# Optimization experiments

Hardware: AMD Instinct MI355X
Metric: run time of the kernel (lower is better)

Reference implementation:

```python
import jax, jax.numpy as jnp
import numpy as np

# dims
B, S, H = 2, 256, 1024          # batch, global seq, global hidden
BH, NH = 384, 8                  # byte_hidden, num heads
HD = BH // NH                    # head dim = 48
P = 4                            # num_global_proj (seed byte positions)
S_C = 12                         # byte decode steps (= target.shape[2])
L = 4                            # num_byte_decoder_layers
V = 258                          # byte vocab (256 bytes + pad 256 + eos 257)
T = P + S_C
EOS = 257
SCALE = 1.0 / np.sqrt(HD)


def setup_inputs() -> dict:
    key = jax.random.key(0)
    ks = jax.random.split(key, 12)
    w = lambda k, shp: jax.random.normal(k, shp, jnp.float32) * 0.02
    return {
        "x": jax.random.normal(ks[0], (B, S, H), jnp.float32),
        "target": jax.random.randint(ks[1], (B, S, S_C), 0, V),
        "Wproj": w(ks[2], (H, P * BH)),
        "attn_norm": jnp.ones((L, BH), jnp.float32),
        "Wq": w(ks[3], (L, BH, BH)),
        "Wk": w(ks[4], (L, BH, BH)),
        "Wv": w(ks[5], (L, BH, BH)),
        "Wo": w(ks[6], (L, BH, BH)),
        "ffn_norm": jnp.ones((L, BH), jnp.float32),
        "W1": w(ks[7], (L, BH, 4 * BH)),
        "W2": w(ks[8], (L, 4 * BH, BH)),
        "Wlm": w(ks[9], (BH, V)),
    }


def _rms(x, g):
    return x * jax.lax.rsqrt(jnp.mean(x * x, -1, keepdims=True) + 1e-5) * g


def _block(x, kc, vc, pos, an, Wq, Wk, Wv, Wo, fn, W1, W2, causal):
    # x: [N, Lq, BH]; kc/vc: [N, T, NH, HD] KV caches; pos: static write offset
    N, Lq, _ = x.shape
    h = _rms(x, an)
    q = (h @ Wq).reshape(N, Lq, NH, HD)
    k = (h @ Wk).reshape(N, Lq, NH, HD)
    v = (h @ Wv).reshape(N, Lq, NH, HD)
    kc = jax.lax.dynamic_update_slice(kc, k, (0, pos, 0, 0))
    vc = jax.lax.dynamic_update_slice(vc, v, (0, pos, 0, 0))
    nk = pos + Lq
    sc = jnp.einsum('nqhd,nkhd->nhqk', q, kc[:, :nk]) * SCALE
    if causal:
        mask = jnp.arange(nk)[None, :] <= (pos + jnp.arange(Lq))[:, None]
        sc = jnp.where(mask[None, None], sc, jnp.float32(-1e30))
    p = jax.nn.softmax(sc, axis=-1)
    o = jnp.einsum('nhqk,nkhd->nqhd', p, vc[:, :nk]).reshape(N, Lq, BH)
    x = x + o @ Wo
    x = x + jax.nn.gelu(_rms(x, fn) @ W1, approximate=False) @ W2
    return x, kc, vc


def _forward(x, Wproj, attn_norm, Wq, Wk, Wv, Wo, ffn_norm, W1, W2, Wlm):
    N = B * S
    x0 = (x.reshape(N, H) @ Wproj).reshape(N, P, BH)
    x_out = jnp.zeros((N, T, BH), x0.dtype).at[:, :P].set(x0)
    kc = [jnp.zeros((N, T, NH, HD), x0.dtype) for _ in range(L)]
    vc = [jnp.zeros((N, T, NH, HD), x0.dtype) for _ in range(L)]
    finished = jnp.zeros((N,), bool)
    for i in range(S_C):
        if i == 0:
            pos, xi, causal = 0, x_out[:, :P], True          # prefill seed bytes
        else:
            pos, xi, causal = P + i - 1, x_out[:, P + i - 1:P + i], False  # decode 1 token
        for l in range(L):
            xi, kc[l], vc[l] = _block(xi, kc[l], vc[l], pos,
                                      attn_norm[l], Wq[l], Wk[l], Wv[l], Wo[l],
                                      ffn_norm[l], W1[l], W2[l], causal)
        gen = xi[:, -1]                                       # [N, BH]
        unf = ~finished
        # scatter only unfinished streams back (finished stay zero, as in torch)
        x_out = x_out.at[:, P + i].set(jnp.where(unf[:, None], gen, jnp.float32(0.0)))
        finished = finished | (unf & (jnp.argmax(gen, -1) == EOS))
    return x_out.reshape(B, S, T, BH)[:, :, P:, :] @ Wlm      # [B,S,S_C,V]


def reference(x, target, Wproj, attn_norm, Wq, Wk, Wv, Wo, ffn_norm, W1, W2, Wlm):
    del target  # only sets S_c (static here)
    return _forward(x, Wproj, attn_norm, Wq, Wk, Wv, Wo, ffn_norm, W1, W2, Wlm)
```

## Files before the change

kernel.cpp:

```cpp
#include <hip/hip_runtime.h>
#include <hip/hip_bf16.h>


constexpr int H_IN  = 1024;
constexpr int BH    = 384;
constexpr int NH    = 8;
constexpr int HD    = 48;
constexpr int PP    = 4;
constexpr int S_CNT = 12;
constexpr int NL    = 4;
constexpr int NV    = 258;
constexpr int TT    = 16;
constexpr int NSEQ  = 512;
constexpr int EOS_I = 257;
constexpr int NTH   = 768;
constexpr float RSCALE = 0.14433756729740646f;

typedef _Float16 h2 __attribute__((ext_vector_type(2)));
typedef _Float16 h8 __attribute__((ext_vector_type(8)));

union W16 { h8 v8; h2 h[4]; _Float16 e[8]; };

template<int N> struct IC { static constexpr int value = N; };

__device__ __forceinline__ float fdot2(h2 a, h2 b, float c) {
#if __has_builtin(__builtin_amdgcn_fdot2)
  return __builtin_amdgcn_fdot2(a, b, c, false);
#else
  return c + (float)a.x * (float)b.x + (float)a.y * (float)b.y;
#endif
}

__global__ __launch_bounds__(256)
void pack8_kernel(const float* __restrict__ src, h8* __restrict__ dst, int C) {
  int c  = blockIdx.x * 256 + threadIdx.x;
  int j8 = blockIdx.y;
  if (c < C) {
    h8 v;
    #pragma unroll
    for (int r = 0; r < 8; r++) v[r] = (_Float16)src[(size_t)(8 * j8 + r) * C + c];
    dst[(size_t)j8 * C + c] = v;
  }
}

__global__ __launch_bounds__(NTH)
void decoder_kernel(const float* __restrict__ x,
                    const h8* __restrict__ Wproj8,
                    const float* __restrict__ attn_norm,
                    const h8* __restrict__ Wq8,
                    const h8* __restrict__ Wk8,
                    const h8* __restrict__ Wv8,
                    const h8* __restrict__ Wo8,
                    const float* __restrict__ ffn_norm,
                    const h8* __restrict__ W18,
                    const h8* __restrict__ W28,
                    const h8* __restrict__ Wlm8,
                    float* __restrict__ out,
                    _Float16* __restrict__ kbuf,
                    _Float16* __restrict__ vbuf)
{
  __shared__ float xs[2][4][BH];
  __shared__ __align__(16) _Float16 hh[2][4][BH];
  __shared__ __align__(16) _Float16 qh[2][4][BH];
  __shared__ __align__(16) _Float16 oh[2][4][BH];
  __shared__ __align__(16) _Float16 xh[2][H_IN];
  __shared__ __align__(16) _Float16 genh[2][BH];
  __shared__ float sc[2][NH][4][TT];
  __shared__ union Scr {
    float qkvp[3][2][4][BH];
    float wop[2][4][BH];
    struct { __align__(16) _Float16 f1h[2][4][4*BH];
             float w2p[2][4][BH]; } ffn;
  } scr;
  __shared__ float redsum[4][12];
  __shared__ float redv[12];
  __shared__ int   redi[12];
  __shared__ int   amx[2];
  __shared__ int   fin[2];

  const int tid = threadIdx.x;
  const int kg  = tid / BH;
  const int col = tid - kg * BH;
  const int sq  = kg;
  const int wid = tid >> 6;
  const int seq0 = blockIdx.x * 2;

  if (tid < 2) fin[tid] = 0;

  for (int s = 0; s < 2; s++) {
    const size_t base = (size_t)(seq0 + s) * H_IN;
    for (int j = tid; j < H_IN; j += NTH) xh[s][j] = (_Float16)x[base + j];
  }
  __syncthreads();
  {
    float acc[2][2] = {};
    for (int j8 = 0; j8 < H_IN / 8; j8 += 4) {
      W16 w0[4], w1[4];
      #pragma unroll
      for (int u = 0; u < 4; u++) {
        w0[u].v8 = Wproj8[(size_t)(j8 + u) * (PP * BH) + tid];
        w1[u].v8 = Wproj8[(size_t)(j8 + u) * (PP * BH) + tid + NTH];
      }
      #pragma unroll
      for (int u = 0; u < 4; u++)
        #pragma unroll
        for (int s = 0; s < 2; s++) {
          W16 hv; hv.v8 = *(const h8*)&xh[s][(j8 + u) * 8];
          #pragma unroll
          for (int r = 0; r < 4; r++) {
            acc[s][0] = fdot2(hv.h[r], w0[u].h[r], acc[s][0]);
            acc[s][1] = fdot2(hv.h[r], w1[u].h[r], acc[s][1]);
          }
        }
    }
    const int m0 = tid / BH, cc = tid % BH;
    for (int s = 0; s < 2; s++) {
      xs[s][m0][cc]     = acc[s][0];
      xs[s][m0 + 2][cc] = acc[s][1];
    }
  }
  __syncthreads();

  auto layers = [&](auto ntc, int pos, bool causal) {
    constexpr int NT = decltype(ntc)::value;
    const int nk = pos + NT;
    for (int l = 0; l < NL; l++) {
      {
        #pragma unroll
        for (int tok = 0; tok < NT; tok++) {
          float r = xs[sq][tok][col]; r *= r;
          #pragma unroll
          for (int off = 32; off; off >>= 1) r += __shfl_down(r, off, 64);
          if ((tid & 63) == 0) redsum[tok][wid] = r;
        }
        __syncthreads();
        const int b = sq * 6;
        #pragma unroll
        for (int tok = 0; tok < NT; tok++) {
          float ss = redsum[tok][b] + redsum[tok][b+1] + redsum[tok][b+2] +
                     redsum[tok][b+3] + redsum[tok][b+4] + redsum[tok][b+5];
          float sca = rsqrtf(ss * (1.0f / BH) + 1e-5f);
          hh[sq][tok][col] = (_Float16)(xs[sq][tok][col] * sca * attn_norm[l * BH + col]);
        }
        __syncthreads();
      }
      {
        const size_t wb = ((size_t)l * 48 + kg * 24) * BH + col;
        float aq[2][NT] = {}, ak[2][NT] = {}, av[2][NT] = {};
        for (int j8 = 0; j8 < 24; j8 += 4) {
          W16 wq[4], wk[4], wv[4];
          #pragma unroll
          for (int u = 0; u < 4; u++) {
            wq[u].v8 = Wq8[wb + (size_t)(j8 + u) * BH];
            wk[u].v8 = Wk8[wb + (size_t)(j8 + u) * BH];
            wv[u].v8 = Wv8[wb + (size_t)(j8 + u) * BH];
          }
          #pragma unroll
          for (int u = 0; u < 4; u++)
            #pragma unroll
            for (int s = 0; s < 2; s++)
              #pragma unroll
              for (int tok = 0; tok < NT; tok++) {
                W16 hv; hv.v8 = *(const h8*)&hh[s][tok][(kg * 24 + j8 + u) * 8];
                #pragma unroll
                for (int r = 0; r < 4; r++) {
                  aq[s][tok] = fdot2(hv.h[r], wq[u].h[r], aq[s][tok]);
                  ak[s][tok] = fdot2(hv.h[r], wk[u].h[r], ak[s][tok]);
                  av[s][tok] = fdot2(hv.h[r], wv[u].h[r], av[s][tok]);
                }
              }
        }
        if (kg == 1) {
          #pragma unroll
          for (int s = 0; s < 2; s++)
            #pragma unroll
            for (int tok = 0; tok < NT; tok++) {
              scr.qkvp[0][s][tok][col] = aq[s][tok];
              scr.qkvp[1][s][tok][col] = ak[s][tok];
              scr.qkvp[2][s][tok][col] = av[s][tok];
            }
        }
        __syncthreads();
        if (kg == 0) {
          #pragma unroll
          for (int s = 0; s < 2; s++) {
            const size_t cb = (((size_t)(seq0 + s) * NL + l) * TT + pos) * BH + col;
            #pragma unroll
            for (int tok = 0; tok < NT; tok++) {
              qh[s][tok][col] = (_Float16)(aq[s][tok] + scr.qkvp[0][s][tok][col]);
              kbuf[cb + (size_t)tok * BH] = (_Float16)(ak[s][tok] + scr.qkvp[1][s][tok][col]);
              vbuf[cb + (size_t)tok * BH] = (_Float16)(av[s][tok] + scr.qkvp[2][s][tok][col]);
            }
          }
        }
        __syncthreads();
      }
      {
        const int nu = 2 * NH * NT * nk;
        if (tid < nu) {
          int s = tid / (NH * NT * nk), r = tid % (NH * NT * nk);
          int h = r / (NT * nk); int r2 = r % (NT * nk);
          int qi = r2 / nk, j = r2 % nk;
          float d;
          if (causal && j > pos + qi) d = -1e30f;
          else {
            const h8* kp8 = (const h8*)(kbuf + (((size_t)(seq0 + s) * NL + l) * TT + j) * BH + h * HD);
            W16 kk[6];
            #pragma unroll
            for (int c = 0; c < 6; c++) kk[c].v8 = kp8[c];
            d = 0.f;
            #pragma unroll
            for (int c = 0; c < 6; c++)
              #pragma unroll
              for (int e = 0; e < 8; e++)
                d += (float)qh[s][qi][h * HD + c * 8 + e] * (float)kk[c].e[e];
            d *= RSCALE;
          }
          sc[s][h][qi][j] = d;
        }
      }
      __syncthreads();
      {
        const int nr = 2 * NH * NT;
        if (tid < nr) {
          int s = tid / (NH * NT), r = tid % (NH * NT);
          int h = r / NT, qi = r % NT;
          float m = -3.0e38f;
          for (int j = 0; j < nk; j++) m = fmaxf(m, sc[s][h][qi][j]);
          float den = 0.f;
          for (int j = 0; j < nk; j++) {
            float e = expf(sc[s][h][qi][j] - m);
            sc[s][h][qi][j] = e; den += e;
          }
          float inv = 1.0f / den;
          for (int j = 0; j < nk; j++) sc[s][h][qi][j] *= inv;
        }
      }
      __syncthreads();
      {
        const size_t vb = (((size_t)(seq0 + sq) * NL + l) * TT) * BH + col;
        const int h = col / HD;
        #pragma unroll
        for (int tok = 0; tok < NT; tok++) {
          float acc = 0.f;
          int j = 0;
          for (; j + 4 <= nk; j += 4) {
            float v0 = (float)vbuf[vb + (size_t)(j + 0) * BH];
            float v1 = (float)vbuf[vb + (size_t)(j + 1) * BH];
            float v2 = (float)vbuf[vb + (size_t)(j + 2) * BH];
            float v3 = (float)vbuf[vb + (size_t)(j + 3) * BH];
            acc += sc[sq][h][tok][j] * v0 + sc[sq][h][tok][j+1] * v1 +
                   sc[sq][h][tok][j+2] * v2 + sc[sq][h][tok][j+3] * v3;
          }
          for (; j < nk; j++)
            acc += sc[sq][h][tok][j] * (float)vbuf[vb + (size_t)j * BH];
          oh[sq][tok][col] = (_Float16)acc;
        }
      }
      __syncthreads();
      {
        const size_t wb = ((size_t)l * 48 + kg * 24) * BH + col;
        float ao[2][NT] = {};
        for (int j8 = 0; j8 < 24; j8 += 8) {
          W16 w[8];
          #pragma unroll
          for (int u = 0; u < 8; u++) w[u].v8 = Wo8[wb + (size_t)(j8 + u) * BH];
          #pragma unroll
          for (int u = 0; u < 8; u++)
            #pragma unroll
            for (int s = 0; s < 2; s++)
              #pragma unroll
              for (int tok = 0; tok < NT; tok++) {
                W16 hv; hv.v8 = *(const h8*)&oh[s][tok][(kg * 24 + j8 + u) * 8];
                #pragma unroll
                for (int r = 0; r < 4; r++)
                  ao[s][tok] = fdot2(hv.h[r], w[u].h[r], ao[s][tok]);
              }
        }
        if (kg == 1) {
          #pragma unroll
          for (int s = 0; s < 2; s++)
            #pragma unroll
            for (int tok = 0; tok < NT; tok++) scr.wop[s][tok][col] = ao[s][tok];
        }
        __syncthreads();
        if (kg == 0) {
          #pragma unroll
          for (int s = 0; s < 2; s++)
            #pragma unroll
            for (int tok = 0; tok < NT; tok++)
              xs[s][tok][col] += ao[s][tok] + scr.wop[s][tok][col];
        }
        __syncthreads();
      }
      {
        #pragma unroll
        for (int tok = 0; tok < NT; tok++) {
          float r = xs[sq][tok][col]; r *= r;
          #pragma unroll
          for (int off = 32; off; off >>= 1) r += __shfl_down(r, off, 64);
          if ((tid & 63) == 0) redsum[tok][wid] = r;
        }
        __syncthreads();
        const int b = sq * 6;
        #pragma unroll
        for (int tok = 0; tok < NT; tok++) {
          float ss = redsum[tok][b] + redsum[tok][b+1] + redsum[tok][b+2] +
                     redsum[tok][b+3] + redsum[tok][b+4] + redsum[tok][b+5];
          float sca = rsqrtf(ss * (1.0f / BH) + 1e-5f);
          hh[sq][tok][col] = (_Float16)(xs[sq][tok][col] * sca * ffn_norm[l * BH + col]);
        }
        __syncthreads();
      }
      {
        float a1[2][NT][2] = {};
        for (int j8 = 0; j8 < 48; j8 += 4) {
          W16 w0[4], w1[4];
          #pragma unroll
          for (int u = 0; u < 4; u++) {
            w0[u].v8 = W18[((size_t)(l * 48 + j8 + u)) * (4 * BH) + tid];
            w1[u].v8 = W18[((size_t)(l * 48 + j8 + u)) * (4 * BH) + tid + NTH];
          }
          #pragma unroll
          for (int u = 0; u < 4; u++)
            #pragma unroll
            for (int s = 0; s < 2; s++)
              #pragma unroll
              for (int t = 0; t < NT; t++) {
                W16 hv; hv.v8 = *(const h8*)&hh[s][t][(j8 + u) * 8];
                #pragma unroll
                for (int r = 0; r < 4; r++) {
                  a1[s][t][0] = fdot2(hv.h[r], w0[u].h[r], a1[s][t][0]);
                  a1[s][t][1] = fdot2(hv.h[r], w1[u].h[r], a1[s][t][1]);
                }
              }
        }
        #pragma unroll
        for (int s = 0; s < 2; s++)
          #pragma unroll
          for (int t = 0; t < NT; t++) {
            float z0 = a1[s][t][0], z1 = a1[s][t][1];
            scr.ffn.f1h[s][t][tid]       = (_Float16)(0.5f * z0 * (1.0f + erff(z0 * 0.7071067811865476f)));
            scr.ffn.f1h[s][t][tid + NTH] = (_Float16)(0.5f * z1 * (1.0f + erff(z1 * 0.7071067811865476f)));
          }
        __syncthreads();
        {
          float a2[2][NT] = {};
          for (int j8 = 0; j8 < 96; j8 += 8) {
            W16 w[8];
            #pragma unroll
            for (int u = 0; u < 8; u++)
              w[u].v8 = W28[((size_t)(l * 192 + kg * 96 + j8 + u)) * BH + col];
            #pragma unroll
            for (int u = 0; u < 8; u++)
              #pragma unroll
              for (int s = 0; s < 2; s++)
                #pragma unroll
                for (int t = 0; t < NT; t++) {
                  W16 fv; fv.v8 = *(const h8*)&scr.ffn.f1h[s][t][(kg * 96 + j8 + u) * 8];
                  #pragma unroll
                  for (int r = 0; r < 4; r++)
                    a2[s][t] = fdot2(fv.h[r], w[u].h[r], a2[s][t]);
                }
          }
          if (kg == 1) {
            #pragma unroll
            for (int s = 0; s < 2; s++)
              #pragma unroll
              for (int t = 0; t < NT; t++) scr.ffn.w2p[s][t][col] = a2[s][t];
          }
          __syncthreads();
          if (kg == 0) {
            #pragma unroll
            for (int s = 0; s < 2; s++)
              #pragma unroll
              for (int t = 0; t < NT; t++)
                xs[s][t][col] += a2[s][t] + scr.ffn.w2p[s][t][col];
          }
          __syncthreads();
        }
      }
    }
  };

  for (int i = 0; i < S_CNT; i++) {
    int grow;
    if (i == 0) { layers(IC<4>{}, 0, true);           grow = 3; }
    else        { layers(IC<1>{}, PP + i - 1, false); grow = 0; }

    {
      float v = xs[sq][grow][col]; int idx = col;
      #pragma unroll
      for (int off = 32; off; off >>= 1) {
        float v2 = __shfl_down(v, off, 64); int i2 = __shfl_down(idx, off, 64);
        if (v2 > v || (v2 == v && i2 < idx)) { v = v2; idx = i2; }
      }
      if ((tid & 63) == 0) { redv[wid] = v; redi[wid] = idx; }
      __syncthreads();
      if (col == 0) {
        const int b = sq * 6;
        float bv = redv[b]; int bi = redi[b];
        for (int w = 1; w < 6; w++)
          if (redv[b + w] > bv || (redv[b + w] == bv && redi[b + w] < bi)) {
            bv = redv[b + w]; bi = redi[b + w];
          }
        amx[sq] = bi;
      }
      genh[sq][col] = (_Float16)xs[sq][grow][col];
      __syncthreads();
    }
    if (col < NV) {
      float acc = 0.f;
      for (int j8 = 0; j8 < 48; j8 += 8) {
        W16 w[8];
        #pragma unroll
        for (int u = 0; u < 8; u++) w[u].v8 = Wlm8[(size_t)(j8 + u) * NV + col];
        #pragma unroll
        for (int u = 0; u < 8; u++) {
          W16 gv; gv.v8 = *(const h8*)&genh[sq][(j8 + u) * 8];
          #pragma unroll
          for (int r = 0; r < 4; r++) acc = fdot2(gv.h[r], w[u].h[r], acc);
        }
      }
      out[((size_t)(seq0 + sq) * S_CNT + i) * NV + col] = fin[sq] ? 0.0f : acc;
    }
    __syncthreads();
    {
      float gv = xs[sq][grow][col];
      xs[sq][0][col] = fin[sq] ? 0.0f : gv;
    }
    __syncthreads();
    if (tid < 2 && amx[tid] == EOS_I) fin[tid] = 1;
    __syncthreads();
  }
}

extern "C" void kernel_launch(void* const* d_in, const int* in_sizes, int n_in,
                              void* d_out, int out_size, void* d_ws, size_t ws_size,
                              hipStream_t stream) {
  const float* x     = (const float*)d_in[0];
  const float* Wproj = (const float*)d_in[2];
  const float* an    = (const float*)d_in[3];
  const float* Wq    = (const float*)d_in[4];
  const float* Wk    = (const float*)d_in[5];
  const float* Wv    = (const float*)d_in[6];
  const float* Wo    = (const float*)d_in[7];
  const float* fn    = (const float*)d_in[8];
  const float* W1    = (const float*)d_in[9];
  const float* W2    = (const float*)d_in[10];
  const float* Wlm   = (const float*)d_in[11];
  float* out = (float*)d_out;
  (void)ws_size; (void)in_sizes; (void)n_in; (void)out_size;

  h8* w = (h8*)d_ws;
  const int n_proj = (H_IN / 8) * (PP * BH);
  const int n_qkvo = NL * (BH / 8) * BH;
  const int n_w1   = NL * (BH / 8) * (4 * BH);
  const int n_w2   = NL * (4 * BH / 8) * BH;
  const int n_lm   = (BH / 8) * NV;
  h8* Wproj_p = w;  w += n_proj;
  h8* Wq_p    = w;  w += n_qkvo;
  h8* Wk_p    = w;  w += n_qkvo;
  h8* Wv_p    = w;  w += n_qkvo;
  h8* Wo_p    = w;  w += n_qkvo;
  h8* W1_p    = w;  w += n_w1;
  h8* W2_p    = w;  w += n_w2;
  h8* Wlm_p   = w;  w += n_lm;
  const size_t kv_elems = (size_t)NSEQ * NL * TT * BH;
  _Float16* kbuf = (_Float16*)w;
  _Float16* vbuf = kbuf + kv_elems;

  auto pack = [&](const float* src, h8* dst, int R, int C) {
    dim3 grid((C + 255) / 256, R / 8);
    pack8_kernel<<<grid, 256, 0, stream>>>(src, dst, C);
  };
  pack(Wproj, Wproj_p, H_IN,        PP * BH);
  pack(Wq,    Wq_p,    NL * BH,     BH);
  pack(Wk,    Wk_p,    NL * BH,     BH);
  pack(Wv,    Wv_p,    NL * BH,     BH);
  pack(Wo,    Wo_p,    NL * BH,     BH);
  pack(W1,    W1_p,    NL * BH,     4 * BH);
  pack(W2,    W2_p,    NL * 4 * BH, BH);
  pack(Wlm,   Wlm_p,   BH,          NV);

  decoder_kernel<<<NSEQ / 2, NTH, 0, stream>>>(
      x, Wproj_p, an, Wq_p, Wk_p, Wv_p, Wo_p, fn, W1_p, W2_p, Wlm_p, out, kbuf, vbuf);
}
```

Before: 2.433 ms.

## Fold RMSNorm gains into packed weights and defer normalization scale past matmuls

The RMSNorm gain vectors are multiplied into the fp16-packed Wq/Wk/Wv/W1 rows at pack time. The per-token rsqrt scale is applied after the QKV and W1 matmuls instead of before, and the attention 1/sqrt(d) factor is folded into q. Sum-of-squares reductions are fused into the residual updates, which removes two norm phases and their barriers per layer. The sequential tail (argmax, LM head, feedback) is merged into fewer sync phases. Because the unnormalized residual is now cast to fp16 before the matmul, precision and overflow risk goes up if activations grow large.

```diff
diff --git a/kernel.cpp b/kernel.cpp
--- a/kernel.cpp
+++ b/kernel.cpp
@@ -32,13 +32,18 @@
 }
 
 __global__ __launch_bounds__(256)
-void pack8_kernel(const float* __restrict__ src, h8* __restrict__ dst, int C) {
+void pack8_kernel(const float* __restrict__ src, const float* __restrict__ g,
+                  h8* __restrict__ dst, int C) {
   int c  = blockIdx.x * 256 + threadIdx.x;
   int j8 = blockIdx.y;
   if (c < C) {
     h8 v;
     #pragma unroll
-    for (int r = 0; r < 8; r++) v[r] = (_Float16)src[(size_t)(8 * j8 + r) * C + c];
+    for (int r = 0; r < 8; r++) {
+      int row = 8 * j8 + r;
+      float s = g ? g[row] : 1.0f;
+      v[r] = (_Float16)(src[(size_t)row * C + c] * s);
+    }
     dst[(size_t)j8 * C + c] = v;
   }
 }
@@ -46,12 +51,10 @@
 __global__ __launch_bounds__(NTH)
 void decoder_kernel(const float* __restrict__ x,
                     const h8* __restrict__ Wproj8,
-                    const float* __restrict__ attn_norm,
                     const h8* __restrict__ Wq8,
                     const h8* __restrict__ Wk8,
                     const h8* __restrict__ Wv8,
                     const h8* __restrict__ Wo8,
-                    const float* __restrict__ ffn_norm,
                     const h8* __restrict__ W18,
                     const h8* __restrict__ W28,
                     const h8* __restrict__ Wlm8,
@@ -60,22 +63,20 @@
                     _Float16* __restrict__ vbuf)
 {
   __shared__ float xs[2][4][BH];
-  __shared__ __align__(16) _Float16 hh[2][4][BH];
+  __shared__ __align__(16) _Float16 xh[2][4][BH];
   __shared__ __align__(16) _Float16 qh[2][4][BH];
   __shared__ __align__(16) _Float16 oh[2][4][BH];
-  __shared__ __align__(16) _Float16 xh[2][H_IN];
-  __shared__ __align__(16) _Float16 genh[2][BH];
   __shared__ float sc[2][NH][4][TT];
-  __shared__ union Scr {
+  __shared__ __align__(16) union Scr {
     float qkvp[3][2][4][BH];
     float wop[2][4][BH];
     struct { __align__(16) _Float16 f1h[2][4][4*BH];
              float w2p[2][4][BH]; } ffn;
+    __align__(16) _Float16 xin[2][H_IN];
   } scr;
-  __shared__ float redsum[4][12];
+  __shared__ float redsq[2][4][6];
   __shared__ float redv[12];
   __shared__ int   redi[12];
-  __shared__ int   amx[2];
   __shared__ int   fin[2];
 
   const int tid = threadIdx.x;
@@ -83,13 +84,14 @@
   const int col = tid - kg * BH;
   const int sq  = kg;
   const int wid = tid >> 6;
+  const int w6  = wid % 6;
   const int seq0 = blockIdx.x * 2;
 
   if (tid < 2) fin[tid] = 0;
 
   for (int s = 0; s < 2; s++) {
     const size_t base = (size_t)(seq0 + s) * H_IN;
-    for (int j = tid; j < H_IN; j += NTH) xh[s][j] = (_Float16)x[base + j];
+    for (int j = tid; j < H_IN; j += NTH) scr.xin[s][j] = (_Float16)x[base + j];
   }
   __syncthreads();
   {
@@ -105,7 +107,7 @@
       for (int u = 0; u < 4; u++)
         #pragma unroll
         for (int s = 0; s < 2; s++) {
-          W16 hv; hv.v8 = *(const h8*)&xh[s][(j8 + u) * 8];
+          W16 hv; hv.v8 = *(const h8*)&scr.xin[s][(j8 + u) * 8];
           #pragma unroll
           for (int r = 0; r < 4; r++) {
             acc[s][0] = fdot2(hv.h[r], w0[u].h[r], acc[s][0]);
@@ -113,10 +115,17 @@
           }
         }
     }
-    const int m0 = tid / BH, cc = tid % BH;
+    const int m0 = tid / BH, cc = tid - m0 * BH;
+    #pragma unroll
     for (int s = 0; s < 2; s++) {
-      xs[s][m0][cc]     = acc[s][0];
-      xs[s][m0 + 2][cc] = acc[s][1];
+      xs[s][m0][cc]     = acc[s][0];  xh[s][m0][cc]     = (_Float16)acc[s][0];
+      xs[s][m0 + 2][cc] = acc[s][1];  xh[s][m0 + 2][cc] = (_Float16)acc[s][1];
+      float r0 = acc[s][0] * acc[s][0], r1 = acc[s][1] * acc[s][1];
+      #pragma unroll
+      for (int off = 32; off; off >>= 1) {
+        r0 += __shfl_down(r0, off, 64); r1 += __shfl_down(r1, off, 64);
+      }
+      if ((tid & 63) == 0) { redsq[s][m0][w6] = r0; redsq[s][m0 + 2][w6] = r1; }
     }
   }
   __syncthreads();
@@ -126,25 +135,6 @@
     const int nk = pos + NT;
     for (int l = 0; l < NL; l++) {
       {
-        #pragma unroll
-        for (int tok = 0; tok < NT; tok++) {
-          float r = xs[sq][tok][col]; r *= r;
-          #pragma unroll
-          for (int off = 32; off; off >>= 1) r += __shfl_down(r, off, 64);
-          if ((tid & 63) == 0) redsum[tok][wid] = r;
-        }
-        __syncthreads();
-        const int b = sq * 6;
-        #pragma unroll
-        for (int tok = 0; tok < NT; tok++) {
-          float ss = redsum[tok][b] + redsum[tok][b+1] + redsum[tok][b+2] +
-                     redsum[tok][b+3] + redsum[tok][b+4] + redsum[tok][b+5];
-          float sca = rsqrtf(ss * (1.0f / BH) + 1e-5f);
-          hh[sq][tok][col] = (_Float16)(xs[sq][tok][col] * sca * attn_norm[l * BH + col]);
-        }
-        __syncthreads();
-      }
-      {
         const size_t wb = ((size_t)l * 48 + kg * 24) * BH + col;
         float aq[2][NT] = {}, ak[2][NT] = {}, av[2][NT] = {};
         for (int j8 = 0; j8 < 24; j8 += 4) {
@@ -161,7 +151,7 @@
             for (int s = 0; s < 2; s++)
               #pragma unroll
               for (int tok = 0; tok < NT; tok++) {
-                W16 hv; hv.v8 = *(const h8*)&hh[s][tok][(kg * 24 + j8 + u) * 8];
+                W16 hv; hv.v8 = *(const h8*)&xh[s][tok][(kg * 24 + j8 + u) * 8];
                 #pragma unroll
                 for (int r = 0; r < 4; r++) {
                   aq[s][tok] = fdot2(hv.h[r], wq[u].h[r], aq[s][tok]);
@@ -187,9 +177,12 @@
             const size_t cb = (((size_t)(seq0 + s) * NL + l) * TT + pos) * BH + col;
             #pragma unroll
             for (int tok = 0; tok < NT; tok++) {
-              qh[s][tok][col] = (_Float16)(aq[s][tok] + scr.qkvp[0][s][tok][col]);
-              kbuf[cb + (size_t)tok * BH] = (_Float16)(ak[s][tok] + scr.qkvp[1][s][tok][col]);
-              vbuf[cb + (size_t)tok * BH] = (_Float16)(av[s][tok] + scr.qkvp[2][s][tok][col]);
+              float ss = redsq[s][tok][0] + redsq[s][tok][1] + redsq[s][tok][2] +
+                         redsq[s][tok][3] + redsq[s][tok][4] + redsq[s][tok][5];
+              float sca = rsqrtf(ss * (1.0f / BH) + 1e-5f);
+              qh[s][tok][col] = (_Float16)((aq[s][tok] + scr.qkvp[0][s][tok][col]) * sca * RSCALE);
+              kbuf[cb + (size_t)tok * BH] = (_Float16)((ak[s][tok] + scr.qkvp[1][s][tok][col]) * sca);
+              vbuf[cb + (size_t)tok * BH] = (_Float16)((av[s][tok] + scr.qkvp[2][s][tok][col]) * sca);
             }
           }
         }
@@ -214,7 +207,6 @@
               #pragma unroll
               for (int e = 0; e < 8; e++)
                 d += (float)qh[s][qi][h * HD + c * 8 + e] * (float)kk[c].e[e];
-            d *= RSCALE;
           }
           sc[s][h][qi][j] = d;
         }
@@ -288,27 +280,14 @@
           #pragma unroll
           for (int s = 0; s < 2; s++)
             #pragma unroll
-            for (int tok = 0; tok < NT; tok++)
-              xs[s][tok][col] += ao[s][tok] + scr.wop[s][tok][col];
-        }
-        __syncthreads();
-      }
-      {
-        #pragma unroll
-        for (int tok = 0; tok < NT; tok++) {
-          float r = xs[sq][tok][col]; r *= r;
-          #pragma unroll
-          for (int off = 32; off; off >>= 1) r += __shfl_down(r, off, 64);
-          if ((tid & 63) == 0) redsum[tok][wid] = r;
-        }
-        __syncthreads();
-        const int b = sq * 6;
-        #pragma unroll
-        for (int tok = 0; tok < NT; tok++) {
-          float ss = redsum[tok][b] + redsum[tok][b+1] + redsum[tok][b+2] +
-                     redsum[tok][b+3] + redsum[tok][b+4] + redsum[tok][b+5];
-          float sca = rsqrtf(ss * (1.0f / BH) + 1e-5f);
-          hh[sq][tok][col] = (_Float16)(xs[sq][tok][col] * sca * ffn_norm[l * BH + col]);
+            for (int tok = 0; tok < NT; tok++) {
+              float xn = xs[s][tok][col] + ao[s][tok] + scr.wop[s][tok][col];
+              xs[s][tok][col] = xn; xh[s][tok][col] = (_Float16)xn;
+              float r = xn * xn;
+              #pragma unroll
+              for (int off = 32; off; off >>= 1) r += __shfl_down(r, off, 64);
+              if ((tid & 63) == 0) redsq[s][tok][wid] = r;
+            }
         }
         __syncthreads();
       }
@@ -327,7 +306,7 @@
             for (int s = 0; s < 2; s++)
               #pragma unroll
               for (int t = 0; t < NT; t++) {
-                W16 hv; hv.v8 = *(const h8*)&hh[s][t][(j8 + u) * 8];
+                W16 hv; hv.v8 = *(const h8*)&xh[s][t][(j8 + u) * 8];
                 #pragma unroll
                 for (int r = 0; r < 4; r++) {
                   a1[s][t][0] = fdot2(hv.h[r], w0[u].h[r], a1[s][t][0]);
@@ -339,7 +318,10 @@
         for (int s = 0; s < 2; s++)
           #pragma unroll
           for (int t = 0; t < NT; t++) {
-            float z0 = a1[s][t][0], z1 = a1[s][t][1];
+            float ss = redsq[s][t][0] + redsq[s][t][1] + redsq[s][t][2] +
+                       redsq[s][t][3] + redsq[s][t][4] + redsq[s][t][5];
+            float sca = rsqrtf(ss * (1.0f / BH) + 1e-5f);
+            float z0 = a1[s][t][0] * sca, z1 = a1[s][t][1] * sca;
             scr.ffn.f1h[s][t][tid]       = (_Float16)(0.5f * z0 * (1.0f + erff(z0 * 0.7071067811865476f)));
             scr.ffn.f1h[s][t][tid + NTH] = (_Float16)(0.5f * z1 * (1.0f + erff(z1 * 0.7071067811865476f)));
           }
@@ -374,8 +356,14 @@
             #pragma unroll
             for (int s = 0; s < 2; s++)
               #pragma unroll
-              for (int t = 0; t < NT; t++)
-                xs[s][t][col] += a2[s][t] + scr.ffn.w2p[s][t][col];
+              for (int t = 0; t < NT; t++) {
+                float xn = xs[s][t][col] + a2[s][t] + scr.ffn.w2p[s][t][col];
+                xs[s][t][col] = xn; xh[s][t][col] = (_Float16)xn;
+                float r = xn * xn;
+                #pragma unroll
+                for (int off = 32; off; off >>= 1) r += __shfl_down(r, off, 64);
+                if ((tid & 63) == 0) redsq[s][t][wid] = r;
+              }
           }
           __syncthreads();
         }
@@ -389,14 +377,23 @@
     else        { layers(IC<1>{}, PP + i - 1, false); grow = 0; }
 
     {
-      float v = xs[sq][grow][col]; int idx = col;
+      float gen = xs[sq][grow][col];
+      float v = gen; int idx = col;
       #pragma unroll
       for (int off = 32; off; off >>= 1) {
         float v2 = __shfl_down(v, off, 64); int i2 = __shfl_down(idx, off, 64);
         if (v2 > v || (v2 == v && i2 < idx)) { v = v2; idx = i2; }
       }
       if ((tid & 63) == 0) { redv[wid] = v; redi[wid] = idx; }
+      float nxt = fin[sq] ? 0.0f : gen;
+      xs[sq][0][col] = nxt; xh[sq][0][col] = (_Float16)nxt;
+      float r = nxt * nxt;
+      #pragma unroll
+      for (int off = 32; off; off >>= 1) r += __shfl_down(r, off, 64);
+      if ((tid & 63) == 0) redsq[sq][0][w6] = r;
       __syncthreads();
+    }
+    {
       if (col == 0) {
         const int b = sq * 6;
         float bv = redv[b]; int bi = redi[b];
@@ -404,34 +401,25 @@
           if (redv[b + w] > bv || (redv[b + w] == bv && redi[b + w] < bi)) {
             bv = redv[b + w]; bi = redi[b + w];
           }
-        amx[sq] = bi;
-      }
-      genh[sq][col] = (_Float16)xs[sq][grow][col];
+        if (bi == EOS_I) fin[sq] = 1;
+      }
+      if (col < NV) {
+        float acc = 0.f;
+        for (int j8 = 0; j8 < 48; j8 += 8) {
+          W16 w[8];
+          #pragma unroll
+          for (int u = 0; u < 8; u++) w[u].v8 = Wlm8[(size_t)(j8 + u) * NV + col];
+          #pragma unroll
+          for (int u = 0; u < 8; u++) {
+            W16 gv; gv.v8 = *(const h8*)&xh[sq][0][(j8 + u) * 8];
+            #pragma unroll
+            for (int r = 0; r < 4; r++) acc = fdot2(gv.h[r], w[u].h[r], acc);
+          }
+        }
+        out[((size_t)(seq0 + sq) * S_CNT + i) * NV + col] = acc;
+      }
       __syncthreads();
     }
-    if (col < NV) {
-      float acc = 0.f;
-      for (int j8 = 0; j8 < 48; j8 += 8) {
-        W16 w[8];
-        #pragma unroll
-        for (int u = 0; u < 8; u++) w[u].v8 = Wlm8[(size_t)(j8 + u) * NV + col];
-        #pragma unroll
-        for (int u = 0; u < 8; u++) {
-          W16 gv; gv.v8 = *(const h8*)&genh[sq][(j8 + u) * 8];
-          #pragma unroll
-          for (int r = 0; r < 4; r++) acc = fdot2(gv.h[r], w[u].h[r], acc);
-        }
-      }
-      out[((size_t)(seq0 + sq) * S_CNT + i) * NV + col] = fin[sq] ? 0.0f : acc;
-    }
-    __syncthreads();
-    {
-      float gv = xs[sq][grow][col];
-      xs[sq][0][col] = fin[sq] ? 0.0f : gv;
-    }
-    __syncthreads();
-    if (tid < 2 && amx[tid] == EOS_I) fin[tid] = 1;
-    __syncthreads();
   }
 }
 
@@ -470,19 +458,19 @@
   _Float16* kbuf = (_Float16*)w;
   _Float16* vbuf = kbuf + kv_elems;
 
-  auto pack = [&](const float* src, h8* dst, int R, int C) {
+  auto pack = [&](const float* src, const float* g, h8* dst, int R, int C) {
     dim3 grid((C + 255) / 256, R / 8);
-    pack8_kernel<<<grid, 256, 0, stream>>>(src, dst, C);
+    pack8_kernel<<<grid, 256, 0, stream>>>(src, g, dst, C);
   };
-  pack(Wproj, Wproj_p, H_IN,        PP * BH);
-  pack(Wq,    Wq_p,    NL * BH,     BH);
-  pack(Wk,    Wk_p,    NL * BH,     BH);
-  pack(Wv,    Wv_p,    NL * BH,     BH);
-  pack(Wo,    Wo_p,    NL * BH,     BH);
-  pack(W1,    W1_p,    NL * BH,     4 * BH);
-  pack(W2,    W2_p,    NL * 4 * BH, BH);
-  pack(Wlm,   Wlm_p,   BH,          NV);
+  pack(Wproj, nullptr, Wproj_p, H_IN,        PP * BH);
+  pack(Wq,    an,      Wq_p,    NL * BH,     BH);
+  pack(Wk,    an,      Wk_p,    NL * BH,     BH);
+  pack(Wv,    an,      Wv_p,    NL * BH,     BH);
+  pack(Wo,    nullptr, Wo_p,    NL * BH,     BH);
+  pack(W1,    fn,      W1_p,    NL * BH,     4 * BH);
+  pack(W2,    nullptr, W2_p,    NL * 4 * BH, BH);
+  pack(Wlm,   nullptr, Wlm_p,   BH,          NV);
 
   decoder_kernel<<<NSEQ / 2, NTH, 0, stream>>>(
-      x, Wproj_p, an, Wq_p, Wk_p, Wv_p, Wo_p, fn, W1_p, W2_p, Wlm_p, out, kbuf, vbuf);
+      x, Wproj_p, Wq_p, Wk_p, Wv_p, Wo_p, W1_p, W2_p, Wlm_p, out, kbuf, vbuf);
 }
```

Result: no change. 2.425 ms (-0.3%).
